# Performance work log

Hardware: AMD Instinct MI355X
Metric: run time of the kernel (lower is better)

Reference implementation:

```python
import jax, jax.numpy as jnp
import numpy as np

TEMP = 0.5      # init temperature
EPS = 1e-8      # torch CosineSimilarity eps
B = 4096
D = 512


def setup_inputs() -> dict:
    key = jax.random.key(0)
    k1, k2 = jax.random.split(key)
    return {
        "zis": jax.random.normal(k1, (B, D), dtype=jnp.float32),
        "zjs": jax.random.normal(k2, (B, D), dtype=jnp.float32),
    }


def reference(zis, zjs):
    # representations = cat([zjs, zis]) -> [2B, D]
    reps = jnp.concatenate([zjs, zis], axis=0)
    b = zis.shape[0]
    n = 2 * b

    # cosine similarity matrix [2B, 2B]
    norms = jnp.maximum(jnp.linalg.norm(reps, axis=-1, keepdims=True), EPS)
    z = reps / norms
    sim = jnp.matmul(z, z.T) / TEMP

    # positive for row i is sim[i, (i+B) % 2B]; self-similarity is excluded.
    # CE with label 0 over [pos, negatives] == logsumexp over row (minus diag)
    # minus the positive logit, because pos is exactly the masked pair entry.
    idx = jnp.arange(n)
    pair = (idx + b) % n
    pos = sim[idx, pair]
    sim_masked = jnp.where(jnp.eye(n, dtype=bool), -1e9, sim)  # drop diagonal
    per_row = jax.nn.logsumexp(sim_masked, axis=-1) - pos
    # criterion sums, then divides by 2B -> mean
    return jnp.mean(per_row)
```

## Files before the change

kernel.cpp:

```cpp
#include <hip/hip_runtime.h>

#define N_TOT 8192
#define BHALF 4096
#define D_DIM 512
#define BM 128
#define BK 64
#define NTILE 64
#define NBLOCKS 2080

typedef float f32x4 __attribute__((ext_vector_type(4)));
typedef short s16x8 __attribute__((ext_vector_type(8)));

__device__ __forceinline__ unsigned short f2bf(float x) {
    union { float f; unsigned int u; } v; v.f = x;
    unsigned int lsb = (v.u >> 16) & 1u;
    unsigned int r = v.u + 0x7fffu + lsb;
    return (unsigned short)(r >> 16);
}

__global__ __launch_bounds__(256) void normalize_kernel(
    const float* __restrict__ zis, const float* __restrict__ zjs,
    unsigned short* __restrict__ zb, float* __restrict__ rowsum)
{
    if (blockIdx.x < 32) rowsum[blockIdx.x * 256 + threadIdx.x] = 0.0f;
    int wave = threadIdx.x >> 6;
    int lane = threadIdx.x & 63;
    int row  = blockIdx.x * 4 + wave;
    const float* src = (row < BHALF) ? (zjs + (size_t)row * D_DIM)
                                     : (zis + (size_t)(row - BHALF) * D_DIM);
    const float4* src4 = (const float4*)src;
    float4 v0 = src4[lane * 2];
    float4 v1 = src4[lane * 2 + 1];
    float ss = v0.x*v0.x + v0.y*v0.y + v0.z*v0.z + v0.w*v0.w
             + v1.x*v1.x + v1.y*v1.y + v1.z*v1.z + v1.w*v1.w;
    #pragma unroll
    for (int off = 1; off < 64; off <<= 1) ss += __shfl_xor(ss, off);
    float scale = 1.0f / fmaxf(sqrtf(ss), 1e-8f);

    float vals[8] = {v0.x, v0.y, v0.z, v0.w, v1.x, v1.y, v1.z, v1.w};
    unsigned short u[8];
    #pragma unroll
    for (int i = 0; i < 8; ++i) u[i] = f2bf(vals[i] * scale);
    uint4 o;
    o.x = u[0] | ((unsigned)u[1] << 16);
    o.y = u[2] | ((unsigned)u[3] << 16);
    o.z = u[4] | ((unsigned)u[5] << 16);
    o.w = u[6] | ((unsigned)u[7] << 16);
    ((uint4*)(zb + (size_t)row * D_DIM))[lane] = o;
}

__global__ __launch_bounds__(256) void ntxent_tri_kernel(
    const unsigned short* __restrict__ zb, float* __restrict__ rowsum,
    float* __restrict__ pos_ws)
{
    __shared__ unsigned short As[BM * BK];
    __shared__ unsigned short Bs[BM * BK];
    __shared__ float rsum_lds[BM];
    __shared__ float csum_lds[BM];

    const int tid  = threadIdx.x;
    const int wave = tid >> 6;
    const int lane = tid & 63;
    const int cq   = lane & 15;
    const int quad = lane >> 4;
    const int wr   = wave >> 1;
    const int wc   = wave & 1;

    int g = 0, rem = blockIdx.x;
    while (rem >= 64 * g + 36) { rem -= 64 * g + 36; ++g; }
    int I, J;
    if (rem < 64 * g) { I = rem >> 3; J = 8 * g + (rem & 7); }
    else {
        rem -= 64 * g;
        int ii = 0;
        while (rem >= 8 - ii) { rem -= 8 - ii; ++ii; }
        I = 8 * g + ii;
        J = I + rem;
    }
    const int rowbase = I * BM;
    const int colbase = J * BM;
    const bool diagblk = (I == J);
    const bool posblk  = (J == I + NTILE / 2);

    if (tid < BM) { rsum_lds[tid] = 0.0f; csum_lds[tid] = 0.0f; }

    const int r0  = tid >> 3;
    const int c8s = (tid & 7) ^ (r0 & 7);
    const unsigned short* gA[4];
    const unsigned short* gB[4];
    #pragma unroll
    for (int rnd = 0; rnd < 4; ++rnd) {
        int r = rnd * 32 + r0;
        gA[rnd] = zb + (size_t)(rowbase + r) * D_DIM + c8s * 8;
        gB[rnd] = zb + (size_t)(colbase + r) * D_DIM + c8s * 8;
    }

    int aOff[4], aSw[4], bOff[4], bSw[4];
    #pragma unroll
    for (int t = 0; t < 4; ++t) {
        int ra = wr * 64 + t * 16 + cq;
        int rb = wc * 64 + t * 16 + cq;
        aOff[t] = ra * 64; aSw[t] = ra & 7;
        bOff[t] = rb * 64; bSw[t] = rb & 7;
    }

    f32x4 acc[4][4];
    #pragma unroll
    for (int a = 0; a < 4; ++a)
        #pragma unroll
        for (int b = 0; b < 4; ++b)
            acc[a][b] = (f32x4){0.f, 0.f, 0.f, 0.f};

    for (int kc = 0; kc < D_DIM / BK; ++kc) {
        __syncthreads();
        #pragma unroll
        for (int rnd = 0; rnd < 4; ++rnd) {
            __builtin_amdgcn_global_load_lds(
                (const __attribute__((address_space(1))) unsigned int*)gA[rnd],
                (__attribute__((address_space(3))) unsigned int*)&As[(rnd * 256 + tid) * 8],
                16, 0, 0);
            __builtin_amdgcn_global_load_lds(
                (const __attribute__((address_space(1))) unsigned int*)gB[rnd],
                (__attribute__((address_space(3))) unsigned int*)&Bs[(rnd * 256 + tid) * 8],
                16, 0, 0);
            gA[rnd] += BK; gB[rnd] += BK;
        }
        __syncthreads();

        #pragma unroll
        for (int kk = 0; kk < 2; ++kk) {
            s16x8 af[4], bf[4];
            const int c8a = kk * 4 + quad;
            #pragma unroll
            for (int t = 0; t < 4; ++t) {
                af[t] = *(const s16x8*)&As[aOff[t] + ((c8a ^ aSw[t]) << 3)];
                bf[t] = *(const s16x8*)&Bs[bOff[t] + ((c8a ^ bSw[t]) << 3)];
            }
            #pragma unroll
            for (int ar = 0; ar < 4; ++ar)
                #pragma unroll
                for (int bc = 0; bc < 4; ++bc)
                    acc[ar][bc] = __builtin_amdgcn_mfma_f32_16x16x32_bf16(
                        af[ar], bf[bc], acc[ar][bc], 0, 0, 0);
        }
    }

    if (posblk && wc == wr) {
        #pragma unroll
        for (int ar = 0; ar < 4; ++ar)
            #pragma unroll
            for (int reg = 0; reg < 4; ++reg)
                if (cq == quad * 4 + reg) {
                    int gr = rowbase + wr * 64 + ar * 16 + quad * 4 + reg;
                    pos_ws[gr] = acc[ar][ar][reg] * 2.0f;
                }
    }

    #pragma unroll
    for (int ar = 0; ar < 4; ++ar)
        #pragma unroll
        for (int bc = 0; bc < 4; ++bc)
            #pragma unroll
            for (int reg = 0; reg < 4; ++reg)
                acc[ar][bc][reg] = __expf(acc[ar][bc][reg] * 2.0f);
    if (diagblk && wr == wc) {
        #pragma unroll
        for (int ar = 0; ar < 4; ++ar)
            #pragma unroll
            for (int reg = 0; reg < 4; ++reg)
                if (cq == quad * 4 + reg) acc[ar][ar][reg] = 0.0f;
    }

    #pragma unroll
    for (int ar = 0; ar < 4; ++ar) {
        float rs[4];
        #pragma unroll
        for (int reg = 0; reg < 4; ++reg) {
            float v = acc[ar][0][reg] + acc[ar][1][reg] + acc[ar][2][reg] + acc[ar][3][reg];
            v += __shfl_xor(v, 1); v += __shfl_xor(v, 2);
            v += __shfl_xor(v, 4); v += __shfl_xor(v, 8);
            rs[reg] = v;
        }
        if (cq == 0) {
            #pragma unroll
            for (int reg = 0; reg < 4; ++reg)
                atomicAdd(&rsum_lds[wr * 64 + ar * 16 + quad * 4 + reg], rs[reg]);
        }
    }

    if (!diagblk) {
        #pragma unroll
        for (int bc = 0; bc < 4; ++bc) {
            float cs = 0.0f;
            #pragma unroll
            for (int ar = 0; ar < 4; ++ar)
                #pragma unroll
                for (int reg = 0; reg < 4; ++reg)
                    cs += acc[ar][bc][reg];
            cs += __shfl_xor(cs, 16); cs += __shfl_xor(cs, 32);
            if (quad == 0) atomicAdd(&csum_lds[wc * 64 + bc * 16 + cq], cs);
        }
    }

    __syncthreads();
    if (tid < BM) atomicAdd(&rowsum[rowbase + tid], rsum_lds[tid]);
    else if (!diagblk) atomicAdd(&rowsum[colbase + tid - BM], csum_lds[tid - BM]);
}

__global__ __launch_bounds__(256) void finalize_kernel(
    const float* __restrict__ rowsum, const float* __restrict__ pos_ws,
    float* __restrict__ out)
{
    __shared__ float red[4];
    float s = 0.0f;
    for (int r = threadIdx.x; r < N_TOT; r += 256)
        s += __logf(rowsum[r]) - pos_ws[r & (BHALF - 1)];
    #pragma unroll
    for (int off = 1; off < 64; off <<= 1) s += __shfl_xor(s, off);
    int wave = threadIdx.x >> 6, lane = threadIdx.x & 63;
    if (lane == 0) red[wave] = s;
    __syncthreads();
    if (threadIdx.x == 0)
        out[0] = (red[0] + red[1] + red[2] + red[3]) * (1.0f / N_TOT);
}

extern "C" void kernel_launch(void* const* d_in, const int* in_sizes, int n_in,
                              void* d_out, int out_size, void* d_ws, size_t ws_size,
                              hipStream_t stream) {
    const float* zis = (const float*)d_in[0];
    const float* zjs = (const float*)d_in[1];
    float* rowsum = (float*)d_ws;
    float* pos_ws = (float*)d_ws + N_TOT;
    unsigned short* zb = (unsigned short*)((float*)d_ws + N_TOT + BHALF);
    float* out = (float*)d_out;

    normalize_kernel<<<N_TOT / 4, 256, 0, stream>>>(zis, zjs, zb, rowsum);
    ntxent_tri_kernel<<<NBLOCKS, 256, 0, stream>>>(zb, rowsum, pos_ws);
    finalize_kernel<<<1, 256, 0, stream>>>(rowsum, pos_ws, out);
}
```

Baseline: 133.5 us.

## Fuse finalize into tile kernel via last-block atomic counter and reuse LDS

Removes the separate finalize launch. Each tile block increments a global counter after its rowsum atomics, and the last block to arrive computes the log-sum and mean. The reduction scratch now reuses the GEMM tile shared memory, and launch bounds request 5 waves per SIMD to raise occupancy. The cost is an extra fence and global atomic per block, plus a serial tail in the last block, in exchange for one fewer kernel launch.

```diff
diff --git a/kernel.cpp b/kernel.cpp
--- a/kernel.cpp
+++ b/kernel.cpp
@@ -20,9 +20,11 @@
 
 __global__ __launch_bounds__(256) void normalize_kernel(
     const float* __restrict__ zis, const float* __restrict__ zjs,
-    unsigned short* __restrict__ zb, float* __restrict__ rowsum)
+    unsigned short* __restrict__ zb, float* __restrict__ rowsum,
+    unsigned int* __restrict__ ctr)
 {
     if (blockIdx.x < 32) rowsum[blockIdx.x * 256 + threadIdx.x] = 0.0f;
+    if (blockIdx.x == 32 && threadIdx.x == 0) *ctr = 0u;
     int wave = threadIdx.x >> 6;
     int lane = threadIdx.x & 63;
     int row  = blockIdx.x * 4 + wave;
@@ -49,14 +51,14 @@
     ((uint4*)(zb + (size_t)row * D_DIM))[lane] = o;
 }
 
-__global__ __launch_bounds__(256) void ntxent_tri_kernel(
+__global__ __launch_bounds__(256, 5) void ntxent_fused_kernel(
     const unsigned short* __restrict__ zb, float* __restrict__ rowsum,
-    float* __restrict__ pos_ws)
+    float* __restrict__ pos_ws, unsigned int* __restrict__ ctr,
+    float* __restrict__ out)
 {
-    __shared__ unsigned short As[BM * BK];
-    __shared__ unsigned short Bs[BM * BK];
-    __shared__ float rsum_lds[BM];
-    __shared__ float csum_lds[BM];
+    __shared__ unsigned char smem[32 * 1024];
+    unsigned short* As = (unsigned short*)smem;
+    unsigned short* Bs = (unsigned short*)(smem + 16384);
 
     const int tid  = threadIdx.x;
     const int wave = tid >> 6;
@@ -82,8 +84,6 @@
     const bool diagblk = (I == J);
     const bool posblk  = (J == I + NTILE / 2);
 
-    if (tid < BM) { rsum_lds[tid] = 0.0f; csum_lds[tid] = 0.0f; }
-
     const int r0  = tid >> 3;
     const int c8s = (tid & 7) ^ (r0 & 7);
     const unsigned short* gA[4];
@@ -152,7 +152,8 @@
             for (int reg = 0; reg < 4; ++reg)
                 if (cq == quad * 4 + reg) {
                     int gr = rowbase + wr * 64 + ar * 16 + quad * 4 + reg;
-                    pos_ws[gr] = acc[ar][ar][reg] * 2.0f;
+                    __hip_atomic_store(&pos_ws[gr], acc[ar][ar][reg] * 2.0f,
+                                       __ATOMIC_RELAXED, __HIP_MEMORY_SCOPE_AGENT);
                 }
     }
 
@@ -170,6 +171,12 @@
             for (int reg = 0; reg < 4; ++reg)
                 if (cq == quad * 4 + reg) acc[ar][ar][reg] = 0.0f;
     }
+
+    __syncthreads();
+    float* red  = (float*)smem;
+    int*   flag = (int*)(smem + 1024);
+    red[tid] = 0.0f;
+    __syncthreads();
 
     #pragma unroll
     for (int ar = 0; ar < 4; ++ar) {
@@ -184,7 +191,7 @@
         if (cq == 0) {
             #pragma unroll
             for (int reg = 0; reg < 4; ++reg)
-                atomicAdd(&rsum_lds[wr * 64 + ar * 16 + quad * 4 + reg], rs[reg]);
+                atomicAdd(&red[wr * 64 + ar * 16 + quad * 4 + reg], rs[reg]);
         }
     }
 
@@ -198,30 +205,39 @@
                 for (int reg = 0; reg < 4; ++reg)
                     cs += acc[ar][bc][reg];
             cs += __shfl_xor(cs, 16); cs += __shfl_xor(cs, 32);
-            if (quad == 0) atomicAdd(&csum_lds[wc * 64 + bc * 16 + cq], cs);
-        }
-    }
-
-    __syncthreads();
-    if (tid < BM) atomicAdd(&rowsum[rowbase + tid], rsum_lds[tid]);
-    else if (!diagblk) atomicAdd(&rowsum[colbase + tid - BM], csum_lds[tid - BM]);
-}
-
-__global__ __launch_bounds__(256) void finalize_kernel(
-    const float* __restrict__ rowsum, const float* __restrict__ pos_ws,
-    float* __restrict__ out)
-{
-    __shared__ float red[4];
-    float s = 0.0f;
-    for (int r = threadIdx.x; r < N_TOT; r += 256)
-        s += __logf(rowsum[r]) - pos_ws[r & (BHALF - 1)];
-    #pragma unroll
-    for (int off = 1; off < 64; off <<= 1) s += __shfl_xor(s, off);
-    int wave = threadIdx.x >> 6, lane = threadIdx.x & 63;
-    if (lane == 0) red[wave] = s;
-    __syncthreads();
-    if (threadIdx.x == 0)
-        out[0] = (red[0] + red[1] + red[2] + red[3]) * (1.0f / N_TOT);
+            if (quad == 0) atomicAdd(&red[128 + wc * 64 + bc * 16 + cq], cs);
+        }
+    }
+
+    __syncthreads();
+    if (tid < BM) atomicAdd(&rowsum[rowbase + tid], red[tid]);
+    else if (!diagblk) atomicAdd(&rowsum[colbase + tid - BM], red[tid]);
+
+    __threadfence();
+    __syncthreads();
+    if (tid == 0) {
+        unsigned int t = __hip_atomic_fetch_add(ctr, 1u, __ATOMIC_ACQ_REL,
+                                                __HIP_MEMORY_SCOPE_AGENT);
+        *flag = (t == NBLOCKS - 1);
+    }
+    __syncthreads();
+    if (*flag) {
+        float s = 0.0f;
+        for (int r = tid; r < N_TOT; r += 256) {
+            float rsv = __hip_atomic_load(&rowsum[r], __ATOMIC_RELAXED,
+                                          __HIP_MEMORY_SCOPE_AGENT);
+            float pv  = __hip_atomic_load(&pos_ws[r & (BHALF - 1)], __ATOMIC_RELAXED,
+                                          __HIP_MEMORY_SCOPE_AGENT);
+            s += __logf(rsv) - pv;
+        }
+        #pragma unroll
+        for (int off = 1; off < 64; off <<= 1) s += __shfl_xor(s, off);
+        __syncthreads();
+        if (lane == 0) red[wave] = s;
+        __syncthreads();
+        if (tid == 0)
+            out[0] = (red[0] + red[1] + red[2] + red[3]) * (1.0f / N_TOT);
+    }
 }
 
 extern "C" void kernel_launch(void* const* d_in, const int* in_sizes, int n_in,
@@ -231,10 +247,10 @@
     const float* zjs = (const float*)d_in[1];
     float* rowsum = (float*)d_ws;
     float* pos_ws = (float*)d_ws + N_TOT;
-    unsigned short* zb = (unsigned short*)((float*)d_ws + N_TOT + BHALF);
+    unsigned int* ctr = (unsigned int*)((float*)d_ws + N_TOT + BHALF);
+    unsigned short* zb = (unsigned short*)((float*)d_ws + N_TOT + BHALF + 64);
     float* out = (float*)d_out;
 
-    normalize_kernel<<<N_TOT / 4, 256, 0, stream>>>(zis, zjs, zb, rowsum);
-    ntxent_tri_kernel<<<NBLOCKS, 256, 0, stream>>>(zb, rowsum, pos_ws);
-    finalize_kernel<<<1, 256, 0, stream>>>(rowsum, pos_ws, out);
-}
+    normalize_kernel<<<N_TOT / 4, 256, 0, stream>>>(zis, zjs, zb, rowsum, ctr);
+    ntxent_fused_kernel<<<NBLOCKS, 256, 0, stream>>>(zb, rowsum, pos_ws, ctr, out);
+}
```

After: 458.0 us. 243% more time.
